# Kernel tuning notes

Hardware: AMD Instinct MI355X
Metric: run time of the kernel (lower is better)

The kernel has to match this reference:

```python
import jax, jax.numpy as jnp
import numpy as np

B, Q, C, N_PER, GS = 8, 2048, 256, 64, 8
H1, H2 = 256, 64
EPS = 1e-5


def make_grid():
    a = jnp.linspace(-0.1, 0.1, GS)
    gx, gy = jnp.meshgrid(a, a, indexing='ij')  # torch.meshgrid default 'ij'
    return jnp.stack([gx.reshape(-1), gy.reshape(-1)], axis=1)  # (n, 2)


def setup_inputs() -> dict:
    key = jax.random.key(0)
    ks = jax.random.split(key, 10)
    s = lambda k, shp, fan: jax.random.normal(k, shp, jnp.float32) / np.sqrt(fan)
    return {
        'tokens': jax.random.normal(ks[0], (B, Q, C), jnp.float32),
        'grid': make_grid(),
        'Wc': s(ks[1], (C, 3), C), 'bc': jnp.zeros((3,), jnp.float32),
        'W1': s(ks[2], (C + 2, H1), C + 2), 'b1': jnp.zeros((H1,), jnp.float32),
        'gamma1': jnp.ones((H1,), jnp.float32), 'beta1': jnp.zeros((H1,), jnp.float32),
        'W2': s(ks[3], (H1, H2), H1), 'b2': jnp.zeros((H2,), jnp.float32),
        'gamma2': jnp.ones((H2,), jnp.float32), 'beta2': jnp.zeros((H2,), jnp.float32),
        'W3': s(ks[4], (H2, 3), H2), 'b3': jnp.zeros((3,), jnp.float32),
    }


def batchnorm(x, gamma, beta):
    # BatchNorm1d in training mode: stats over batch (B*Q) and length (n) dims,
    # per channel (last axis here).
    mean = jnp.mean(x, axis=(0, 1, 2), keepdims=True)
    var = jnp.var(x, axis=(0, 1, 2), keepdims=True)
    return gamma * (x - mean) * jax.lax.rsqrt(var + EPS) + beta


def reference(tokens, grid, Wc, bc, W1, b1, gamma1, beta1, W2, b2, gamma2, beta2, W3, b3):
    coarse = tokens @ Wc + bc  # (B, Q, 3)
    # conv1 (1x1) on concat([tokens_expanded, grid]) == split matmul + broadcast add;
    # avoids materializing the (B,Q,n,C+2) concat explicitly.
    tok_part = tokens @ W1[:C]                 # (B, Q, H1)
    grid_part = grid @ W1[C:]                  # (n, H1)
    h = tok_part[:, :, None, :] + grid_part[None, None, :, :] + b1  # (B, Q, n, H1)
    h = jax.nn.relu(batchnorm(h, gamma1, beta1))
    h = jnp.einsum('bqnc,cd->bqnd', h, W2) + b2  # (B, Q, n, H2)
    h = jax.nn.relu(batchnorm(h, gamma2, beta2))
    disp = jnp.einsum('bqnc,cd->bqnd', h, W3) + b3  # (B, Q, n, 3)
    fine = (coarse[:, :, None, :] + disp).reshape(B, Q * N_PER, 3)
    return coarse, fine
```

## Files before the change

kernel.cpp:

```cpp
#include <hip/hip_runtime.h>
#include <hip/hip_bf16.h>

#define ROWS 16384
#define C_   256
#define H1_  256
#define H2_  64
#define EPSN 1e-5f

typedef __bf16 bf16x8 __attribute__((ext_vector_type(8)));
typedef __bf16 bf16x4 __attribute__((ext_vector_type(4)));
typedef __bf16 bf16x2 __attribute__((ext_vector_type(2)));
typedef float  f32x4  __attribute__((ext_vector_type(4)));
typedef float  f32x2  __attribute__((ext_vector_type(2)));

__device__ __forceinline__ bf16x2 cvt2(float a, float b) {
#if __has_builtin(__builtin_amdgcn_cvt_pk_bf16_f32)
    return __builtin_bit_cast(bf16x2, __builtin_amdgcn_cvt_pk_bf16_f32(a, b));
#else
    bf16x2 r; r[0] = (__bf16)a; r[1] = (__bf16)b; return r;
#endif
}

__global__ __launch_bounds__(256) void k0_pack(const float* __restrict__ W1,
                                               const float* __restrict__ W2,
                                               const float* __restrict__ W3,
                                               __bf16* __restrict__ W1p,
                                               __bf16* __restrict__ W2p,
                                               __bf16* __restrict__ W3p,
                                               float* __restrict__ zero_base) {
    int idx = blockIdx.x * 256 + threadIdx.x;
    if (idx < 65536) {
        int j = idx & 7, l = (idx >> 3) & 63, rest = idx >> 9;
        int ks = rest & 7, CT = rest >> 3;
        int k = ks * 32 + ((l >> 4) << 3) + j;
        int c = CT * 16 + (l & 15);
        W1p[idx] = (__bf16)W1[k * H1_ + c];
    } else {
        int i2 = idx - 65536;
        int j = i2 & 7, l = (i2 >> 3) & 63, rest = i2 >> 9;
        int ks = rest & 7, CK = rest >> 3;
        int k = ks * 32 + ((l >> 4) << 3) + j;
        int c2 = CK * 16 + (l & 15);
        W2p[i2] = (__bf16)W2[k * H2_ + c2];
    }
    if (idx < 1024) {
        int j = idx & 7, l = (idx >> 3) & 63, ks = idx >> 9;
        int k = ks * 32 + ((l >> 4) << 3) + j;
        int c = l & 15;
        W3p[idx] = (c < 3) ? (__bf16)W3[k * 3 + c] : (__bf16)0.f;
    }
    if (idx < 24576) zero_base[idx] = 0.0f;
}

__device__ __forceinline__ void prep_ctx(const float* __restrict__ grid,
                                         const float* __restrict__ W1,
                                         const float* __restrict__ a1p, int c0,
                                         f32x2* wgx2, f32x2* wgy2, float* A_) {
#pragma unroll
    for (int j = 0; j < 8; ++j) A_[j] = grid[2 * j + 1];
    f32x4 a0 = *(const f32x4*)(a1p + c0), a1h = *(const f32x4*)(a1p + c0 + 4);
    f32x4 x0 = *(const f32x4*)(W1 + C_ * H1_ + c0), x1 = *(const f32x4*)(W1 + C_ * H1_ + c0 + 4);
    f32x4 y0 = *(const f32x4*)(W1 + (C_ + 1) * H1_ + c0), yh = *(const f32x4*)(W1 + (C_ + 1) * H1_ + c0 + 4);
    float av[8] = {a0[0], a0[1], a0[2], a0[3], a1h[0], a1h[1], a1h[2], a1h[3]};
    float wx[8] = {x0[0], x0[1], x0[2], x0[3], x1[0], x1[1], x1[2], x1[3]};
    float wy[8] = {y0[0], y0[1], y0[2], y0[3], yh[0], yh[1], yh[2], yh[3]};
#pragma unroll
    for (int e = 0; e < 4; ++e) {
        wgx2[e][0] = av[2 * e] * wx[2 * e];     wgx2[e][1] = av[2 * e + 1] * wx[2 * e + 1];
        wgy2[e][0] = av[2 * e] * wy[2 * e];     wgy2[e][1] = av[2 * e + 1] * wy[2 * e + 1];
    }
}

__device__ __forceinline__ void stage16(__bf16* __restrict__ y1, int w, int c0, int nh,
                                        const float* __restrict__ a1p,
                                        const float* __restrict__ d1p,
                                        const f32x2* wgx2, const f32x2* wgy2,
                                        const float* A_, f32x4 t0, f32x4 t1) {
    f32x4 a0 = *(const f32x4*)(a1p + c0), a1h = *(const f32x4*)(a1p + c0 + 4);
    f32x4 d0 = *(const f32x4*)(d1p + c0), d1h = *(const f32x4*)(d1p + c0 + 4);
    f32x2 base2[4];
    base2[0][0] = fmaf(a0[0], t0[0], d0[0]);  base2[0][1] = fmaf(a0[1], t0[1], d0[1]);
    base2[1][0] = fmaf(a0[2], t0[2], d0[2]);  base2[1][1] = fmaf(a0[3], t0[3], d0[3]);
    base2[2][0] = fmaf(a1h[0], t1[0], d1h[0]); base2[2][1] = fmaf(a1h[1], t1[1], d1h[1]);
    base2[3][0] = fmaf(a1h[2], t1[2], d1h[2]); base2[3][1] = fmaf(a1h[3], t1[3], d1h[3]);
#pragma unroll
    for (int ih = 0; ih < 2; ++ih) {
        float axs = A_[2 * w + ih];
        f32x2 ax2 = {axs, axs};
        f32x2 tc2[4];
#pragma unroll
        for (int e = 0; e < 4; ++e) tc2[e] = __builtin_elementwise_fma(wgx2[e], ax2, base2[e]);
#pragma unroll
        for (int kk = 0; kk < 4; ++kk) {
            int iy = nh + 2 * kk;
            float ays = A_[iy];
            f32x2 ay2 = {ays, ays};
            f32x2 z = {0.f, 0.f};
            int n = w * 16 + ih * 8 + iy;
            bf16x8 out;
            bf16x2* o2 = (bf16x2*)&out;
#pragma unroll
            for (int e = 0; e < 4; ++e) {
                f32x2 v = __builtin_elementwise_max(
                    __builtin_elementwise_fma(wgy2[e], ay2, tc2[e]), z);
                o2[e] = cvt2(v[0], v[1]);
            }
            *(bf16x8*)(&y1[n * 264 + c0]) = out;
        }
    }
}

__global__ __launch_bounds__(256) void k1a(const float* __restrict__ tokens,
                                           const __bf16* __restrict__ W1p,
                                           const float* __restrict__ Wc,
                                           const float* __restrict__ bc,
                                           float* __restrict__ tokpart,
                                           float* __restrict__ coarse,
                                           float* __restrict__ p1s,
                                           float* __restrict__ p1q) {
    __shared__ __align__(16) __bf16 Al[16 * 264];
    int t = threadIdx.x, w = t >> 6, l = t & 63;
    int quad = l >> 4, col = l & 15;
    int rowbase = (blockIdx.x >> 1) * 16;
    int colhalf = blockIdx.x & 1;
    int slot = blockIdx.x & 31;

    bf16x8 bfr[16];
#pragma unroll
    for (int ctl = 0; ctl < 2; ++ctl)
#pragma unroll
        for (int ks = 0; ks < 8; ++ks) {
            int CT = colhalf * 8 + w * 2 + ctl;
            bfr[ctl * 8 + ks] = *(const bf16x8*)(W1p + (((CT * 8 + ks) * 64 + l) * 8));
        }
    {
        int r = t >> 4, cb = (t & 15) * 16;
        const float* src = tokens + (size_t)(rowbase + r) * C_ + cb;
        f32x4 t0 = *(const f32x4*)(src);
        f32x4 t1 = *(const f32x4*)(src + 4);
        f32x4 t2 = *(const f32x4*)(src + 8);
        f32x4 t3 = *(const f32x4*)(src + 12);
        bf16x8 v0, v1;
        bf16x2* p0 = (bf16x2*)&v0; bf16x2* p1 = (bf16x2*)&v1;
        p0[0] = cvt2(t0[0], t0[1]); p0[1] = cvt2(t0[2], t0[3]);
        p0[2] = cvt2(t1[0], t1[1]); p0[3] = cvt2(t1[2], t1[3]);
        p1[0] = cvt2(t2[0], t2[1]); p1[1] = cvt2(t2[2], t2[3]);
        p1[2] = cvt2(t3[0], t3[1]); p1[3] = cvt2(t3[2], t3[3]);
        *(bf16x8*)(&Al[r * 264 + cb]) = v0;
        *(bf16x8*)(&Al[r * 264 + cb + 8]) = v1;
    }
    __syncthreads();

    bf16x8 af[8];
#pragma unroll
    for (int ks = 0; ks < 8; ++ks)
        af[ks] = *(const bf16x8*)(&Al[col * 264 + ks * 32 + quad * 8]);

#pragma unroll
    for (int ctl = 0; ctl < 2; ++ctl) {
        f32x4 acc = {0.f, 0.f, 0.f, 0.f};
#pragma unroll
        for (int ks = 0; ks < 8; ++ks)
            acc = __builtin_amdgcn_mfma_f32_16x16x32_bf16(af[ks], bfr[ctl * 8 + ks], acc, 0, 0, 0);
        int c = colhalf * 128 + w * 32 + ctl * 16 + col;
        float s = 0.f, q = 0.f;
#pragma unroll
        for (int rr = 0; rr < 4; ++rr) {
            float v = acc[rr];
            tokpart[(size_t)(rowbase + quad * 4 + rr) * C_ + c] = v;
            s += v; q += v * v;
        }
        s += __shfl_xor(s, 16, 64); s += __shfl_xor(s, 32, 64);
        q += __shfl_xor(q, 16, 64); q += __shfl_xor(q, 32, 64);
        if (l < 16) {
            int cc = colhalf * 128 + w * 32 + ctl * 16 + l;
            atomicAdd(p1s + slot * C_ + cc, s);
            atomicAdd(p1q + slot * C_ + cc, q);
        }
    }
    if (colhalf == 0) {
        const f32x4* wcp = (const f32x4*)(Wc + l * 12);
        f32x4 wa = wcp[0], wb = wcp[1], wv = wcp[2];
        float wcl[12] = {wa[0], wa[1], wa[2], wa[3], wb[0], wb[1], wb[2], wb[3],
                         wv[0], wv[1], wv[2], wv[3]};
#pragma unroll
        for (int rr = 0; rr < 4; ++rr) {
            int r = w * 4 + rr;
            bf16x4 tv4 = *(const bf16x4*)(&Al[r * 264 + l * 4]);
            float p[3] = {0.f, 0.f, 0.f};
#pragma unroll
            for (int i = 0; i < 4; ++i) {
                float tvf = (float)tv4[i];
#pragma unroll
                for (int j = 0; j < 3; ++j) p[j] = fmaf(tvf, wcl[i * 3 + j], p[j]);
            }
#pragma unroll
            for (int off = 1; off < 64; off <<= 1)
#pragma unroll
                for (int j = 0; j < 3; ++j) p[j] += __shfl_xor(p[j], off, 64);
            if (l == 0) {
#pragma unroll
                for (int j = 0; j < 3; ++j)
                    coarse[(size_t)(rowbase + r) * 3 + j] = p[j] + bc[j];
            }
        }
    }
}

__global__ void k1b(const float* __restrict__ grid, const float* __restrict__ W1,
                    const float* __restrict__ gamma1, const float* __restrict__ beta1,
                    const float* __restrict__ p1s, const float* __restrict__ p1q,
                    float* __restrict__ a1o, float* __restrict__ d1o) {
    int t = threadIdx.x;
    float S = 0.f, Qq = 0.f;
    for (int s = 0; s < 32; ++s) { S += p1s[s * C_ + t]; Qq += p1q[s * C_ + t]; }
    float mean_t = S / (float)ROWS;
    float var_t = Qq / (float)ROWS - mean_t * mean_t;
    float wx = W1[C_ * H1_ + t];
    float wy = W1[(C_ + 1) * H1_ + t];
    float mg = 0.f, qg = 0.f;
    for (int n = 0; n < 64; ++n) {
        float gv = grid[2 * n] * wx + grid[2 * n + 1] * wy;
        mg += gv; qg += gv * gv;
    }
    mg *= (1.f / 64.f);
    float var_g = qg * (1.f / 64.f) - mg * mg;
    float a1 = gamma1[t] * rsqrtf(var_t + var_g + EPSN);
    a1o[t] = a1;
    d1o[t] = beta1[t] - a1 * (mean_t + mg);
}

template <bool SPILL>
__global__ __launch_bounds__(256) void k2(const float* __restrict__ tokpart,
                                          const float* __restrict__ grid,
                                          const float* __restrict__ W1,
                                          const __bf16* __restrict__ W2p,
                                          const float* __restrict__ a1,
                                          const float* __restrict__ d1,
                                          float* __restrict__ p2s,
                                          float* __restrict__ p2q,
                                          __bf16* __restrict__ h2s) {
    __shared__ __align__(16) __bf16 y1[64 * 264];
    __shared__ __align__(16) __bf16 y2l[SPILL ? 64 * 72 : 8];
    int t = threadIdx.x, w = t >> 6, l = t & 63;
    int quad = l >> 4, col = l & 15;
    int wn = w >> 1, wc = w & 1;
    int c0 = (l & 31) * 8, nh = l >> 5;

    bf16x8 bfr[16];
#pragma unroll
    for (int ck = 0; ck < 2; ++ck)
#pragma unroll
        for (int ks = 0; ks < 8; ++ks)
            bfr[ck * 8 + ks] = *(const bf16x8*)(W2p + ((((wc * 2 + ck) * 8 + ks) * 64 + l) * 8));

    f32x2 wgx2[4], wgy2[4]; float A_[8];
    prep_ctx(grid, W1, a1, c0, wgx2, wgy2, A_);

    float s[2][4] = {}, q[2][4] = {};

    const float* tokbase = tokpart + (size_t)blockIdx.x * 8 * C_;
    f32x4 t0 = *(const f32x4*)(tokbase + c0);
    f32x4 t1 = *(const f32x4*)(tokbase + c0 + 4);

#pragma unroll 1
    for (int r8 = 0; r8 < 8; ++r8) {
        int row = blockIdx.x * 8 + r8;
        int nr = (r8 < 7) ? (r8 + 1) : 7;
        f32x4 n0 = *(const f32x4*)(tokbase + (size_t)nr * C_ + c0);
        f32x4 n1 = *(const f32x4*)(tokbase + (size_t)nr * C_ + c0 + 4);

        stage16(y1, w, c0, nh, a1, d1, wgx2, wgy2, A_, t0, t1);
        __syncthreads();
#pragma unroll
        for (int rt = 0; rt < 2; ++rt) {
            bf16x8 af[8];
#pragma unroll
            for (int ks = 0; ks < 8; ++ks)
                af[ks] = *(const bf16x8*)(&y1[(wn * 32 + rt * 16 + col) * 264 + ks * 32 + quad * 8]);
#pragma unroll
            for (int ck = 0; ck < 2; ++ck) {
                f32x4 acc = {0.f, 0.f, 0.f, 0.f};
#pragma unroll
                for (int ks = 0; ks < 8; ++ks)
                    acc = __builtin_amdgcn_mfma_f32_16x16x32_bf16(bfr[ck * 8 + ks], af[ks], acc, 0, 0, 0);
#pragma unroll
                for (int rr = 0; rr < 4; ++rr) {
                    s[ck][rr] += acc[rr];
                    q[ck][rr] += acc[rr] * acc[rr];
                }
                if constexpr (SPILL) {
                    bf16x4 v; bf16x2* v2 = (bf16x2*)&v;
                    v2[0] = cvt2(acc[0], acc[1]);
                    v2[1] = cvt2(acc[2], acc[3]);
                    *(bf16x4*)(&y2l[(wn * 32 + rt * 16 + col) * 72 + wc * 32 + ck * 16 + quad * 4]) = v;
                }
            }
        }
        __syncthreads();
        if constexpr (SPILL) {
            int n = t >> 2, cb = (t & 3) * 16;
            bf16x8 u0 = *(const bf16x8*)(&y2l[n * 72 + cb]);
            bf16x8 u1 = *(const bf16x8*)(&y2l[n * 72 + cb + 8]);
            __bf16* dst = h2s + (size_t)row * 4096 + t * 16;
            *(bf16x8*)dst = u0;
            *(bf16x8*)(dst + 8) = u1;
        }
        t0 = n0; t1 = n1;
    }
    int slot = ((blockIdx.x << 1) | wn) & 63;
#pragma unroll
    for (int ck = 0; ck < 2; ++ck)
#pragma unroll
        for (int rr = 0; rr < 4; ++rr) {
            float sv = s[ck][rr], qv = q[ck][rr];
            sv += __shfl_xor(sv, 1, 64); sv += __shfl_xor(sv, 2, 64);
            sv += __shfl_xor(sv, 4, 64); sv += __shfl_xor(sv, 8, 64);
            qv += __shfl_xor(qv, 1, 64); qv += __shfl_xor(qv, 2, 64);
            qv += __shfl_xor(qv, 4, 64); qv += __shfl_xor(qv, 8, 64);
            if (col == 0) {
                int c2 = wc * 32 + ck * 16 + quad * 4 + rr;
                atomicAdd(p2s + slot * H2_ + c2, sv);
                atomicAdd(p2q + slot * H2_ + c2, qv);
            }
        }
}

__global__ void k2b(const float* __restrict__ p2s, const float* __restrict__ p2q,
                    const float* __restrict__ gamma2, const float* __restrict__ beta2,
                    float* __restrict__ a2o, float* __restrict__ d2o) {
    int t = threadIdx.x;
    float S = 0.f, Qq = 0.f;
    for (int s = 0; s < 64; ++s) { S += p2s[s * H2_ + t]; Qq += p2q[s * H2_ + t]; }
    const float invN = 1.f / ((float)ROWS * 64.f);
    float mean = S * invN;
    float var = Qq * invN - mean * mean;
    float a2 = gamma2[t] * rsqrtf(var + EPSN);
    a2o[t] = a2;
    d2o[t] = beta2[t] - a2 * mean;
}

__global__ __launch_bounds__(256) void k3s(const __bf16* __restrict__ h2s,
                                           const float* __restrict__ a2,
                                           const float* __restrict__ d2p,
                                           const __bf16* __restrict__ W3p,
                                           const float* __restrict__ b3,
                                           const float* __restrict__ coarse,
                                           float* __restrict__ fine) {
    __shared__ __align__(16) __bf16 y2l[8][64 * 72];
    __shared__ __align__(16) float finebuf[8 * 192];
    int t = threadIdx.x, w = t >> 6, l = t & 63;
    int quad = l >> 4, col = l & 15;

    bf16x8 wfr[2];
#pragma unroll
    for (int ks = 0; ks < 2; ++ks)
        wfr[ks] = *(const bf16x8*)(W3p + ((ks * 64 + l) * 8));

    int n = t >> 2, cb = (t & 3) * 16;
    float a2r[16], d2r[16];
#pragma unroll
    for (int i = 0; i < 16; i += 4) {
        f32x4 av = *(const f32x4*)(a2 + cb + i);
        f32x4 dv = *(const f32x4*)(d2p + cb + i);
#pragma unroll
        for (int e = 0; e < 4; ++e) { a2r[i + e] = av[e]; d2r[i + e] = dv[e]; }
    }
#pragma unroll 1
    for (int r8 = 0; r8 < 8; ++r8) {
        size_t row = (size_t)blockIdx.x * 8 + r8;
        const __bf16* src = h2s + row * 4096 + t * 16;
        bf16x8 u0 = *(const bf16x8*)src;
        bf16x8 u1 = *(const bf16x8*)(src + 8);
        bf16x8 o0, o1;
        bf16x2* p0 = (bf16x2*)&o0; bf16x2* p1 = (bf16x2*)&o1;
#pragma unroll
        for (int e = 0; e < 4; ++e) {
            p0[e] = cvt2(fmaxf(fmaf(a2r[2 * e],     (float)u0[2 * e],     d2r[2 * e]), 0.f),
                         fmaxf(fmaf(a2r[2 * e + 1], (float)u0[2 * e + 1], d2r[2 * e + 1]), 0.f));
            p1[e] = cvt2(fmaxf(fmaf(a2r[8 + 2 * e],     (float)u1[2 * e],     d2r[8 + 2 * e]), 0.f),
                         fmaxf(fmaf(a2r[8 + 2 * e + 1], (float)u1[2 * e + 1], d2r[8 + 2 * e + 1]), 0.f));
        }
        *(bf16x8*)(&y2l[r8][n * 72 + cb]) = o0;
        *(bf16x8*)(&y2l[r8][n * 72 + cb + 8]) = o1;
    }
    __syncthreads();
    float b3v = (col < 3) ? b3[col] : 0.f;
#pragma unroll 1
    for (int r8 = 0; r8 < 8; ++r8) {
        int row = blockIdx.x * 8 + r8;
        bf16x8 af2[2];
#pragma unroll
        for (int ks = 0; ks < 2; ++ks)
            af2[ks] = *(const bf16x8*)(&y2l[r8][(w * 16 + col) * 72 + ks * 32 + quad * 8]);
        f32x4 acc = {0.f, 0.f, 0.f, 0.f};
        acc = __builtin_amdgcn_mfma_f32_16x16x32_bf16(af2[0], wfr[0], acc, 0, 0, 0);
        acc = __builtin_amdgcn_mfma_f32_16x16x32_bf16(af2[1], wfr[1], acc, 0, 0, 0);
        if (col < 3) {
            float cj = coarse[row * 3 + col] + b3v;
#pragma unroll
            for (int rr = 0; rr < 4; ++rr)
                finebuf[r8 * 192 + (w * 16 + quad * 4 + rr) * 3 + col] = acc[rr] + cj;
        }
    }
    __syncthreads();
    {
        float* dst = fine + (size_t)blockIdx.x * 1536;
        const f32x4* fb = (const f32x4*)finebuf;
        *(f32x4*)(dst + 4 * t) = fb[t];
        if (t < 128) *(f32x4*)(dst + 1024 + 4 * t) = fb[256 + t];
    }
}

__global__ __launch_bounds__(256) void k3r(const float* __restrict__ tokpart,
                                           const float* __restrict__ grid,
                                           const float* __restrict__ W1,
                                           const __bf16* __restrict__ W2p,
                                           const float* __restrict__ a1,
                                           const float* __restrict__ d1,
                                           const __bf16* __restrict__ W3p,
                                           const float* __restrict__ a2,
                                           const float* __restrict__ d2p,
                                           const float* __restrict__ b3,
                                           const float* __restrict__ coarse,
                                           float* __restrict__ fine) {
    __shared__ __align__(16) __bf16 y1[64 * 264];
    __shared__ __align__(16) __bf16 y2l[64 * 72];
    __shared__ __align__(16) float finebuf[8 * 192];
    int t = threadIdx.x, w = t >> 6, l = t & 63;
    int quad = l >> 4, col = l & 15;
    int wn = w >> 1, wc = w & 1;
    int c0 = (l & 31) * 8, nh = l >> 5;

    bf16x8 bfr[16];
#pragma unroll
    for (int ck = 0; ck < 2; ++ck)
#pragma unroll
        for (int ks = 0; ks < 8; ++ks)
            bfr[ck * 8 + ks] = *(const bf16x8*)(W2p + ((((wc * 2 + ck) * 8 + ks) * 64 + l) * 8));
    bf16x8 wfr[2];
#pragma unroll
    for (int ks = 0; ks < 2; ++ks)
        wfr[ks] = *(const bf16x8*)(W3p + ((ks * 64 + l) * 8));

    f32x2 wgx2[4], wgy2[4]; float A_[8];
    prep_ctx(grid, W1, a1, c0, wgx2, wgy2, A_);

    float a2v[8], d2v[8];
#pragma unroll
    for (int ck = 0; ck < 2; ++ck)
#pragma unroll
        for (int rr = 0; rr < 4; ++rr) {
            int c2 = wc * 32 + ck * 16 + quad * 4 + rr;
            a2v[ck * 4 + rr] = a2[c2];
            d2v[ck * 4 + rr] = d2p[c2];
        }
    float b3v = (col < 3) ? b3[col] : 0.f;

#pragma unroll 1
    for (int r8 = 0; r8 < 8; ++r8) {
        int row = blockIdx.x * 8 + r8;
        const float* tokrow = tokpart + (size_t)row * C_;
        f32x4 t0 = *(const f32x4*)(tokrow + c0);
        f32x4 t1 = *(const f32x4*)(tokrow + c0 + 4);
        stage16(y1, w, c0, nh, a1, d1, wgx2, wgy2, A_, t0, t1);
        __syncthreads();
#pragma unroll
        for (int rt = 0; rt < 2; ++rt) {
            bf16x8 af[8];
#pragma unroll
            for (int ks = 0; ks < 8; ++ks)
                af[ks] = *(const bf16x8*)(&y1[(wn * 32 + rt * 16 + col) * 264 + ks * 32 + quad * 8]);
#pragma unroll
            for (int ck = 0; ck < 2; ++ck) {
                f32x4 acc = {0.f, 0.f, 0.f, 0.f};
#pragma unroll
                for (int ks = 0; ks < 8; ++ks)
                    acc = __builtin_amdgcn_mfma_f32_16x16x32_bf16(bfr[ck * 8 + ks], af[ks], acc, 0, 0, 0);
                bf16x4 v; bf16x2* v2 = (bf16x2*)&v;
                float y0 = fmaxf(fmaf(a2v[ck * 4 + 0], acc[0], d2v[ck * 4 + 0]), 0.f);
                float y1v = fmaxf(fmaf(a2v[ck * 4 + 1], acc[1], d2v[ck * 4 + 1]), 0.f);
                float y2 = fmaxf(fmaf(a2v[ck * 4 + 2], acc[2], d2v[ck * 4 + 2]), 0.f);
                float y3 = fmaxf(fmaf(a2v[ck * 4 + 3], acc[3], d2v[ck * 4 + 3]), 0.f);
                v2[0] = cvt2(y0, y1v); v2[1] = cvt2(y2, y3);
                *(bf16x4*)(&y2l[(wn * 32 + rt * 16 + col) * 72 + wc * 32 + ck * 16 + quad * 4]) = v;
            }
        }
        __syncthreads();
        bf16x8 af2[2];
#pragma unroll
        for (int ks = 0; ks < 2; ++ks)
            af2[ks] = *(const bf16x8*)(&y2l[(w * 16 + col) * 72 + ks * 32 + quad * 8]);
        f32x4 d2acc = {0.f, 0.f, 0.f, 0.f};
        d2acc = __builtin_amdgcn_mfma_f32_16x16x32_bf16(af2[0], wfr[0], d2acc, 0, 0, 0);
        d2acc = __builtin_amdgcn_mfma_f32_16x16x32_bf16(af2[1], wfr[1], d2acc, 0, 0, 0);
        if (col < 3) {
            float cj = coarse[row * 3 + col] + b3v;
#pragma unroll
            for (int rr = 0; rr < 4; ++rr)
                finebuf[r8 * 192 + (w * 16 + quad * 4 + rr) * 3 + col] = d2acc[rr] + cj;
        }
    }
    __syncthreads();
    {
        float* dst = fine + (size_t)blockIdx.x * 1536;
        const f32x4* fb = (const f32x4*)finebuf;
        *(f32x4*)(dst + 4 * t) = fb[t];
        if (t < 128) *(f32x4*)(dst + 1024 + 4 * t) = fb[256 + t];
    }
}

extern "C" void kernel_launch(void* const* d_in, const int* in_sizes, int n_in,
                              void* d_out, int out_size, void* d_ws, size_t ws_size,
                              hipStream_t stream) {
    (void)in_sizes; (void)n_in; (void)out_size;
    const float* tokens = (const float*)d_in[0];
    const float* grid   = (const float*)d_in[1];
    const float* Wc     = (const float*)d_in[2];
    const float* bc     = (const float*)d_in[3];
    const float* W1     = (const float*)d_in[4];
    const float* gamma1 = (const float*)d_in[6];
    const float* beta1  = (const float*)d_in[7];
    const float* W2     = (const float*)d_in[8];
    const float* gamma2 = (const float*)d_in[10];
    const float* beta2  = (const float*)d_in[11];
    const float* W3     = (const float*)d_in[12];
    const float* b3     = (const float*)d_in[13];

    char* ws = (char*)d_ws;
    __bf16* W1p     = (__bf16*)(ws);
    __bf16* W2p     = (__bf16*)(ws + 131072);
    float*  p1s     = (float*)(ws + 163840);
    float*  p1q     = (float*)(ws + 196608);
    float*  p2s     = (float*)(ws + 229376);
    float*  p2q     = (float*)(ws + 245760);
    float*  a1      = (float*)(ws + 262144);
    float*  d1      = (float*)(ws + 263168);
    float*  a2      = (float*)(ws + 264192);
    float*  d2p     = (float*)(ws + 264448);
    __bf16* W3p     = (__bf16*)(ws + 264704);
    float*  tokpart = (float*)(ws + 266752);
    __bf16* h2s     = (__bf16*)(ws + 17043968);

    const size_t SPILL_NEED = 17043968ull + 134217728ull;
    bool spill = ws_size >= SPILL_NEED;

    float* coarse = (float*)d_out;
    float* fine   = (float*)d_out + (size_t)ROWS * 3;

    k0_pack<<<320, 256, 0, stream>>>(W1, W2, W3, W1p, W2p, W3p, p1s);
    k1a<<<2048, 256, 0, stream>>>(tokens, W1p, Wc, bc, tokpart, coarse, p1s, p1q);
    k1b<<<1, 256, 0, stream>>>(grid, W1, gamma1, beta1, p1s, p1q, a1, d1);
    if (spill) {
        k2<true><<<ROWS / 8, 256, 0, stream>>>(tokpart, grid, W1, W2p, a1, d1, p2s, p2q, h2s);
        k2b<<<1, 64, 0, stream>>>(p2s, p2q, gamma2, beta2, a2, d2p);
        k3s<<<ROWS / 8, 256, 0, stream>>>(h2s, a2, d2p, W3p, b3, coarse, fine);
    } else {
        k2<false><<<ROWS / 8, 256, 0, stream>>>(tokpart, grid, W1, W2p, a1, d1, p2s, p2q, h2s);
        k2b<<<1, 64, 0, stream>>>(p2s, p2q, gamma2, beta2, a2, d2p);
        k3r<<<ROWS / 8, 256, 0, stream>>>(tokpart, grid, W1, W2p, a1, d1, W3p, a2, d2p, b3, coarse, fine);
    }
}
```

Before: 210.2 us.

## XOR-swizzle LDS tiles and spill h2 in MFMA fragment order

Replaces the padded LDS layouts (row strides 264/72) with unpadded XOR-swizzled layouts for the y1 and y2 tiles, which cuts LDS footprint and is meant to avoid bank conflicts on the 16-byte fragment reads. The h2 spill now goes straight from MFMA accumulators to global memory in fragment order, dropping the y2l staging buffer and its extra LDS round trip. The consumer kernel reads in that same fragment order and re-swizzles into LDS. It also moves a barrier inside the per-row loop of the fused kernel, which adds synchronisation but fixes reuse of y1 across iterations.

```diff
diff --git a/kernel.cpp b/kernel.cpp
--- a/kernel.cpp
+++ b/kernel.cpp
@@ -78,6 +78,7 @@
                                         const float* A_, f32x4 t0, f32x4 t1) {
     f32x4 a0 = *(const f32x4*)(a1p + c0), a1h = *(const f32x4*)(a1p + c0 + 4);
     f32x4 d0 = *(const f32x4*)(d1p + c0), d1h = *(const f32x4*)(d1p + c0 + 4);
+    int chunk = c0 >> 3;
     f32x2 base2[4];
     base2[0][0] = fmaf(a0[0], t0[0], d0[0]);  base2[0][1] = fmaf(a0[1], t0[1], d0[1]);
     base2[1][0] = fmaf(a0[2], t0[2], d0[2]);  base2[1][1] = fmaf(a0[3], t0[3], d0[3]);
@@ -105,7 +106,7 @@
                     __builtin_elementwise_fma(wgy2[e], ay2, tc2[e]), z);
                 o2[e] = cvt2(v[0], v[1]);
             }
-            *(bf16x8*)(&y1[n * 264 + c0]) = out;
+            *(bf16x8*)(&y1[n * 256 + ((chunk ^ iy) << 3)]) = out;
         }
     }
 }
@@ -240,12 +241,12 @@
                                           float* __restrict__ p2s,
                                           float* __restrict__ p2q,
                                           __bf16* __restrict__ h2s) {
-    __shared__ __align__(16) __bf16 y1[64 * 264];
-    __shared__ __align__(16) __bf16 y2l[SPILL ? 64 * 72 : 8];
+    __shared__ __align__(16) __bf16 y1[64 * 256];
     int t = threadIdx.x, w = t >> 6, l = t & 63;
     int quad = l >> 4, col = l & 15;
     int wn = w >> 1, wc = w & 1;
     int c0 = (l & 31) * 8, nh = l >> 5;
+    int sw = col & 7;
 
     bf16x8 bfr[16];
 #pragma unroll
@@ -274,10 +275,11 @@
         __syncthreads();
 #pragma unroll
         for (int rt = 0; rt < 2; ++rt) {
+            int rowb = (wn * 32 + rt * 16 + col) * 256;
             bf16x8 af[8];
 #pragma unroll
             for (int ks = 0; ks < 8; ++ks)
-                af[ks] = *(const bf16x8*)(&y1[(wn * 32 + rt * 16 + col) * 264 + ks * 32 + quad * 8]);
+                af[ks] = *(const bf16x8*)(&y1[rowb + (((ks * 4 + quad) ^ sw) << 3)]);
 #pragma unroll
             for (int ck = 0; ck < 2; ++ck) {
                 f32x4 acc = {0.f, 0.f, 0.f, 0.f};
@@ -293,19 +295,12 @@
                     bf16x4 v; bf16x2* v2 = (bf16x2*)&v;
                     v2[0] = cvt2(acc[0], acc[1]);
                     v2[1] = cvt2(acc[2], acc[3]);
-                    *(bf16x4*)(&y2l[(wn * 32 + rt * 16 + col) * 72 + wc * 32 + ck * 16 + quad * 4]) = v;
+                    *(bf16x4*)(h2s + (size_t)row * 4096 +
+                               ((w * 2 + rt) * 2 + ck) * 256 + l * 4) = v;
                 }
             }
         }
         __syncthreads();
-        if constexpr (SPILL) {
-            int n = t >> 2, cb = (t & 3) * 16;
-            bf16x8 u0 = *(const bf16x8*)(&y2l[n * 72 + cb]);
-            bf16x8 u1 = *(const bf16x8*)(&y2l[n * 72 + cb + 8]);
-            __bf16* dst = h2s + (size_t)row * 4096 + t * 16;
-            *(bf16x8*)dst = u0;
-            *(bf16x8*)(dst + 8) = u1;
-        }
         t0 = n0; t1 = n1;
     }
     int slot = ((blockIdx.x << 1) | wn) & 63;
@@ -347,52 +342,64 @@
                                            const float* __restrict__ b3,
                                            const float* __restrict__ coarse,
                                            float* __restrict__ fine) {
-    __shared__ __align__(16) __bf16 y2l[8][64 * 72];
+    __shared__ __align__(16) __bf16 y2l[8][64 * 64];
     __shared__ __align__(16) float finebuf[8 * 192];
     int t = threadIdx.x, w = t >> 6, l = t & 63;
     int quad = l >> 4, col = l & 15;
+    int wn = w >> 1, wc = w & 1;
+    int sw = col & 7;
 
     bf16x8 wfr[2];
 #pragma unroll
     for (int ks = 0; ks < 2; ++ks)
         wfr[ks] = *(const bf16x8*)(W3p + ((ks * 64 + l) * 8));
 
-    int n = t >> 2, cb = (t & 3) * 16;
-    float a2r[16], d2r[16];
-#pragma unroll
-    for (int i = 0; i < 16; i += 4) {
-        f32x4 av = *(const f32x4*)(a2 + cb + i);
-        f32x4 dv = *(const f32x4*)(d2p + cb + i);
-#pragma unroll
-        for (int e = 0; e < 4; ++e) { a2r[i + e] = av[e]; d2r[i + e] = dv[e]; }
-    }
+    float a2v[8], d2v[8];
+#pragma unroll
+    for (int ck = 0; ck < 2; ++ck)
+#pragma unroll
+        for (int rr = 0; rr < 4; ++rr) {
+            int c2 = wc * 32 + ck * 16 + quad * 4 + rr;
+            a2v[ck * 4 + rr] = a2[c2];
+            d2v[ck * 4 + rr] = d2p[c2];
+        }
+
 #pragma unroll 1
     for (int r8 = 0; r8 < 8; ++r8) {
         size_t row = (size_t)blockIdx.x * 8 + r8;
-        const __bf16* src = h2s + row * 4096 + t * 16;
-        bf16x8 u0 = *(const bf16x8*)src;
-        bf16x8 u1 = *(const bf16x8*)(src + 8);
-        bf16x8 o0, o1;
-        bf16x2* p0 = (bf16x2*)&o0; bf16x2* p1 = (bf16x2*)&o1;
-#pragma unroll
-        for (int e = 0; e < 4; ++e) {
-            p0[e] = cvt2(fmaxf(fmaf(a2r[2 * e],     (float)u0[2 * e],     d2r[2 * e]), 0.f),
-                         fmaxf(fmaf(a2r[2 * e + 1], (float)u0[2 * e + 1], d2r[2 * e + 1]), 0.f));
-            p1[e] = cvt2(fmaxf(fmaf(a2r[8 + 2 * e],     (float)u1[2 * e],     d2r[8 + 2 * e]), 0.f),
-                         fmaxf(fmaf(a2r[8 + 2 * e + 1], (float)u1[2 * e + 1], d2r[8 + 2 * e + 1]), 0.f));
-        }
-        *(bf16x8*)(&y2l[r8][n * 72 + cb]) = o0;
-        *(bf16x8*)(&y2l[r8][n * 72 + cb + 8]) = o1;
+        const __bf16* src = h2s + row * 4096 + l * 4;
+        bf16x4 u[2][2];
+#pragma unroll
+        for (int rt = 0; rt < 2; ++rt)
+#pragma unroll
+            for (int ck = 0; ck < 2; ++ck)
+                u[rt][ck] = *(const bf16x4*)(src + ((w * 2 + rt) * 2 + ck) * 256);
+#pragma unroll
+        for (int rt = 0; rt < 2; ++rt) {
+            int n = wn * 32 + rt * 16 + col;
+#pragma unroll
+            for (int ck = 0; ck < 2; ++ck) {
+                float y0 = fmaxf(fmaf(a2v[ck * 4 + 0], (float)u[rt][ck][0], d2v[ck * 4 + 0]), 0.f);
+                float y1v = fmaxf(fmaf(a2v[ck * 4 + 1], (float)u[rt][ck][1], d2v[ck * 4 + 1]), 0.f);
+                float y2 = fmaxf(fmaf(a2v[ck * 4 + 2], (float)u[rt][ck][2], d2v[ck * 4 + 2]), 0.f);
+                float y3 = fmaxf(fmaf(a2v[ck * 4 + 3], (float)u[rt][ck][3], d2v[ck * 4 + 3]), 0.f);
+                bf16x4 v; bf16x2* v2 = (bf16x2*)&v;
+                v2[0] = cvt2(y0, y1v); v2[1] = cvt2(y2, y3);
+                int chunk = wc * 4 + ck * 2 + (quad >> 1);
+                *(bf16x4*)(&y2l[r8][n * 64 + ((chunk ^ sw) << 3) + (quad & 1) * 4]) = v;
+            }
+        }
     }
     __syncthreads();
     float b3v = (col < 3) ? b3[col] : 0.f;
 #pragma unroll 1
     for (int r8 = 0; r8 < 8; ++r8) {
         int row = blockIdx.x * 8 + r8;
+        int rowb = (w * 16 + col) * 64;
         bf16x8 af2[2];
 #pragma unroll
         for (int ks = 0; ks < 2; ++ks)
-            af2[ks] = *(const bf16x8*)(&y2l[r8][(w * 16 + col) * 72 + ks * 32 + quad * 8]);
+            af2[ks] = *(const bf16x8*)(&y2l[r8][rowb + (((ks * 4 + quad) ^ sw) << 3)]);
         f32x4 acc = {0.f, 0.f, 0.f, 0.f};
         acc = __builtin_amdgcn_mfma_f32_16x16x32_bf16(af2[0], wfr[0], acc, 0, 0, 0);
         acc = __builtin_amdgcn_mfma_f32_16x16x32_bf16(af2[1], wfr[1], acc, 0, 0, 0);
@@ -424,13 +431,14 @@
                                            const float* __restrict__ b3,
                                            const float* __restrict__ coarse,
                                            float* __restrict__ fine) {
-    __shared__ __align__(16) __bf16 y1[64 * 264];
+    __shared__ __align__(16) __bf16 y1[64 * 256];
     __shared__ __align__(16) __bf16 y2l[64 * 72];
     __shared__ __align__(16) float finebuf[8 * 192];
     int t = threadIdx.x, w = t >> 6, l = t & 63;
     int quad = l >> 4, col = l & 15;
     int wn = w >> 1, wc = w & 1;
     int c0 = (l & 31) * 8, nh = l >> 5;
+    int sw = col & 7;
 
     bf16x8 bfr[16];
 #pragma unroll
@@ -467,10 +475,11 @@
         __syncthreads();
 #pragma unroll
         for (int rt = 0; rt < 2; ++rt) {
+            int rowb = (wn * 32 + rt * 16 + col) * 256;
             bf16x8 af[8];
 #pragma unroll
             for (int ks = 0; ks < 8; ++ks)
-                af[ks] = *(const bf16x8*)(&y1[(wn * 32 + rt * 16 + col) * 264 + ks * 32 + quad * 8]);
+                af[ks] = *(const bf16x8*)(&y1[rowb + (((ks * 4 + quad) ^ sw) << 3)]);
 #pragma unroll
             for (int ck = 0; ck < 2; ++ck) {
                 f32x4 acc = {0.f, 0.f, 0.f, 0.f};
@@ -500,8 +509,8 @@
             for (int rr = 0; rr < 4; ++rr)
                 finebuf[r8 * 192 + (w * 16 + quad * 4 + rr) * 3 + col] = d2acc[rr] + cj;
         }
-    }
-    __syncthreads();
+        __syncthreads();
+    }
     {
         float* dst = fine + (size_t)blockIdx.x * 1536;
         const f32x4* fb = (const f32x4*)finebuf;
```

Measured after the change: 203.5 us. 3.2% less time.
